# Performance work log

Hardware: AMD Instinct MI355X
Metric: run time of the kernel (lower is better)

## Reference

```python
import jax, jax.numpy as jnp
import numpy as np

Z_WHAT = 64      # z_what latent size
DEC = 64         # decoded object patch size
IMG = 128        # output canvas size (ssd_config.DATA.SHAPE[0])
HID = 1024       # what-decoder hidden size
FEATURE_MAPS = [4, 2, 1]
BOXES_PER_LOC = [2, 2, 2]
B = 16


def build_indices():
    # Faithful port of Decoder.reconstruction_indices
    idx = []
    img_idx = last = 0
    for fm, bpl in zip(FEATURE_MAPS, BOXES_PER_LOC):
        for f in range(fm * fm):
            img_idx = last + f
            idx.append(np.full(bpl, img_idx, dtype=np.int32))
        last = img_idx + 1
    return np.concatenate(idx)


def setup_inputs() -> dict:
    key = jax.random.key(0)
    ks = jax.random.split(key, 6)
    idx = build_indices()
    N = idx.shape[0]            # 42 boxes
    NL = int(idx.max()) + 1     # 21 locations
    z_present = jax.random.randint(ks[4], (B, N, 1), 0, 2, jnp.int32)
    z_present = z_present.at[:, 0, 0].set(1)  # ensure >=1 present per image
    return {
        "z_what": jax.random.normal(ks[0], (B, NL, Z_WHAT), jnp.float32),
        "z_where": jax.random.uniform(ks[1], (B, N, 4), jnp.float32, 0.05, 0.95),
        "z_depth": jax.random.normal(ks[2], (B, NL, 1), jnp.float32),
        "w1": jax.random.normal(ks[3], (Z_WHAT, HID), jnp.float32) * 0.05,
        "b1": jnp.zeros((HID,), jnp.float32),
        "w2": jax.random.normal(ks[5], (HID, 3 * DEC * DEC), jnp.float32) * 0.05,
        "b2": jnp.zeros((3 * DEC * DEC,), jnp.float32),
        "z_present": z_present,
        "indices": jnp.asarray(idx),
    }


def _sample_one(img, px, py):
    # Bilinear grid-sample (zeros padding, align_corners=False) of one
    # [3,S,S] patch at pixel coords px, py of shape [H,W].
    S = img.shape[-1]
    x0 = jnp.floor(px)
    y0 = jnp.floor(py)
    wx = px - x0
    wy = py - y0
    x0i = x0.astype(jnp.int32)
    y0i = y0.astype(jnp.int32)

    def gather(xi, yi):
        valid = (xi >= 0) & (xi < S) & (yi >= 0) & (yi < S)
        v = img[:, jnp.clip(yi, 0, S - 1), jnp.clip(xi, 0, S - 1)]
        return v * valid[None].astype(img.dtype)

    return (gather(x0i, y0i) * ((1 - wx) * (1 - wy))[None]
            + gather(x0i + 1, y0i) * (wx * (1 - wy))[None]
            + gather(x0i, y0i + 1) * ((1 - wx) * wy)[None]
            + gather(x0i + 1, y0i + 1) * (wx * wy)[None])


def _forward(z_what, z_where, z_depth, w1, b1, w2, b2, z_present, indices):
    Bb, NL, D = z_what.shape
    N = indices.shape[0]
    # index_select: expand per-location latents to per-box
    zw = jnp.take(z_what, indices, axis=1)          # [B,N,D]
    zd = jnp.take(z_depth, indices, axis=1)[..., 0]  # [B,N]

    # WhatDecoder: MLP -> sigmoid -> [B*N,3,DEC,DEC] object patches
    h = jax.nn.relu(zw.reshape(-1, D) @ w1 + b1)
    dec = jax.nn.sigmoid(h @ w2 + b2).reshape(-1, 3, DEC, DEC)

    # WhereTransformer: place each patch into IMG x IMG canvas via
    # inverse-affine STN from z_where = (cx, cy, w, h) in [0,1].
    zwf = z_where.reshape(-1, 4)
    cx, cy, w, hh = zwf[:, 0], zwf[:, 1], zwf[:, 2], zwf[:, 3]
    t = (jnp.arange(IMG, dtype=z_what.dtype) + 0.5) / IMG * 2.0 - 1.0
    xt = t[None, :]  # [1,IMG]
    yt = t[:, None]  # [IMG,1]
    xs = (xt[None] - (2 * cx - 1)[:, None, None]) / jnp.maximum(w, 1e-6)[:, None, None]
    ys = (yt[None] - (2 * cy - 1)[:, None, None]) / jnp.maximum(hh, 1e-6)[:, None, None]
    px = ((xs + 1) * DEC - 1) / 2  # [B*N,IMG,IMG]
    py = ((ys + 1) * DEC - 1) / 2
    trans = jax.vmap(_sample_one)(dec, px, py).reshape(Bb, N, 3, IMG, IMG)

    # Masked softmax over depth == padded softmax with -inf starter in the
    # original: absent objects get exactly zero merge weight.
    masked = jnp.where(z_present[..., 0] == 1, zd, -jnp.inf)
    wgt = jax.nn.softmax(masked, axis=1)  # [B,N]
    return jnp.einsum('bn,bnchw->bchw', wgt, trans)


def reference(z_what, z_where, z_depth, w1, b1, w2, b2, z_present, indices):
    return _forward(z_what, z_where, z_depth, w1, b1, w2, b2, z_present, indices)
```

## Files before the change

kernel.cpp:

```cpp
#include <hip/hip_runtime.h>

#define B_    16
#define NL    21
#define NG    42
#define ZW    64
#define HID   1024
#define DECW  64
#define IMG   128
#define NOUT  12288
#define MROWS 336
#define MPAD  384

typedef __bf16 bf16x8 __attribute__((ext_vector_type(8)));
typedef float f32x4 __attribute__((ext_vector_type(4)));
typedef unsigned short ushort8v __attribute__((ext_vector_type(8)));
typedef unsigned short ushort4v __attribute__((ext_vector_type(4)));

static __device__ __forceinline__ unsigned short f2bf(float f) {
    union { float f; unsigned int u; } v; v.f = f;
    unsigned int r = v.u + 0x7fffu + ((v.u >> 16) & 1u);
    return (unsigned short)(r >> 16);
}

__global__ __launch_bounds__(256) void k0_w2_transpose(const float* __restrict__ w2,
                                                       unsigned short* __restrict__ w2t) {
    __shared__ float tile[64][65];
    const int nt = blockIdx.x;
    const int kt = blockIdx.y;
    const int t  = threadIdx.x;
    const int n0 = nt * 64, k0 = kt * 64;
    #pragma unroll
    for (int i = 0; i < 4; ++i) {
        int lin = i * 256 + t;
        int kr  = lin >> 4;
        int nc  = (lin & 15) << 2;
        float4 v = *reinterpret_cast<const float4*>(w2 + (size_t)(k0 + kr) * NOUT + n0 + nc);
        tile[kr][nc + 0] = v.x; tile[kr][nc + 1] = v.y;
        tile[kr][nc + 2] = v.z; tile[kr][nc + 3] = v.w;
    }
    __syncthreads();
    #pragma unroll
    for (int i = 0; i < 4; ++i) {
        int lin = i * 256 + t;
        int nc  = lin >> 4;
        int kc  = (lin & 15) << 2;
        ushort4v r;
        r.x = f2bf(tile[kc + 0][nc]);
        r.y = f2bf(tile[kc + 1][nc]);
        r.z = f2bf(tile[kc + 2][nc]);
        r.w = f2bf(tile[kc + 3][nc]);
        *reinterpret_cast<ushort4v*>(w2t + (size_t)(n0 + nc) * HID + k0 + kc) = r;
    }
}

__global__ __launch_bounds__(256) void k1_h(const float* __restrict__ z_what,
                                            const float* __restrict__ w1,
                                            const float* __restrict__ b1,
                                            unsigned short* __restrict__ h) {
    const int r = blockIdx.x, t = threadIdx.x;
    if (r >= MROWS) {
        #pragma unroll
        for (int i = 0; i < 4; ++i) h[(size_t)r * HID + t + i * 256] = 0;
        return;
    }
    __shared__ float zs[ZW];
    if (t < ZW) zs[t] = z_what[(size_t)r * ZW + t];
    __syncthreads();
    float acc[4];
    #pragma unroll
    for (int i = 0; i < 4; ++i) acc[i] = b1[t + i * 256];
    for (int k = 0; k < ZW; ++k) {
        float z = zs[k];
        const float* wr = w1 + (size_t)k * HID + t;
        acc[0] = fmaf(z, wr[0],   acc[0]);
        acc[1] = fmaf(z, wr[256], acc[1]);
        acc[2] = fmaf(z, wr[512], acc[2]);
        acc[3] = fmaf(z, wr[768], acc[3]);
    }
    #pragma unroll
    for (int i = 0; i < 4; ++i)
        h[(size_t)r * HID + t + i * 256] = f2bf(acc[i] > 0.f ? acc[i] : 0.f);
}

__global__ void k3_params(const float* __restrict__ z_where,
                          const float* __restrict__ z_depth,
                          const int* __restrict__ z_present,
                          const int* __restrict__ indices,
                          float* __restrict__ params) {
    const int b = blockIdx.x, t = threadIdx.x;
    const bool valid = t < NG;
    int idx  = valid ? indices[t] : 0;
    int pres = valid ? z_present[b * NG + t] : 0;
    float zd = z_depth[b * NL + idx];
    const bool on = valid && (pres == 1);
    float val = on ? zd : -__builtin_inff();
    float m = val;
    #pragma unroll
    for (int off = 32; off; off >>= 1) m = fmaxf(m, __shfl_xor(m, off));
    float e = on ? __expf(val - m) : 0.f;
    float s = e;
    #pragma unroll
    for (int off = 32; off; off >>= 1) s += __shfl_xor(s, off);
    if (valid) {
        float wn = e / s;
        const float* zw = z_where + (size_t)(b * NG + t) * 4;
        float cx = zw[0], cy = zw[1], ww = zw[2], hh = zw[3];
        float wm = fmaxf(ww, 1e-6f), hm = fmaxf(hh, 1e-6f);
        float Ax = 32.f / wm, Ay = 32.f / hm;
        float Bx = 31.5f - (2.f * cx - 1.f) * Ax;
        float By = 31.5f - (2.f * cy - 1.f) * Ay;
        float* p = params + (size_t)(b * NG + t) * 8;
        p[0] = wn; p[1] = Ax; p[2] = Bx; p[3] = Ay; p[4] = By;
        p[5] = __int_as_float(b * NL + idx);
    }
}

__global__ __launch_bounds__(256) void k2_gemm(const unsigned short* __restrict__ h,
                                               const unsigned short* __restrict__ w2t,
                                               const float* __restrict__ b2,
                                               float* __restrict__ dec) {
    __shared__ unsigned short As[64 * 64];
    __shared__ unsigned short Bs[128 * 64];
    const int t    = threadIdx.x;
    const int bn   = blockIdx.x;
    const int bm   = blockIdx.y;
    const int row0 = bm * 64, col0 = bn * 128;
    const int lane = t & 63, wid = t >> 6;
    const int wr = (wid >> 1) * 32, wc = (wid & 1) * 64;

    f32x4 acc[2][4];
    const f32x4 zero = {0.f, 0.f, 0.f, 0.f};
    #pragma unroll
    for (int m = 0; m < 2; ++m)
        #pragma unroll
        for (int n = 0; n < 4; ++n) acc[m][n] = zero;

    for (int k0 = 0; k0 < HID; k0 += 64) {
        #pragma unroll
        for (int rnd = 0; rnd < 2; ++rnd) {
            int ci  = rnd * 256 + t;
            int row = ci >> 3;
            int bir = (ci & 7) << 4;
            ushort8v v = *reinterpret_cast<const ushort8v*>(
                h + (size_t)(row0 + row) * HID + k0 + (bir >> 1));
            int dst = row * 128 + (bir ^ ((row & 7) << 4));
            *reinterpret_cast<ushort8v*>(reinterpret_cast<char*>(As) + dst) = v;
        }
        #pragma unroll
        for (int rnd = 0; rnd < 4; ++rnd) {
            int ci  = rnd * 256 + t;
            int col = ci >> 3;
            int bir = (ci & 7) << 4;
            ushort8v v = *reinterpret_cast<const ushort8v*>(
                w2t + (size_t)(col0 + col) * HID + k0 + (bir >> 1));
            int dst = col * 128 + (bir ^ ((col & 7) << 4));
            *reinterpret_cast<ushort8v*>(reinterpret_cast<char*>(Bs) + dst) = v;
        }
        __syncthreads();
        #pragma unroll
        for (int ks = 0; ks < 2; ++ks) {
            const int kb = ks * 64 + ((lane >> 4) << 4);
            bf16x8 a[2], bb[4];
            #pragma unroll
            for (int m = 0; m < 2; ++m) {
                int row = wr + m * 16 + (lane & 15);
                int ad  = row * 128 + (kb ^ ((row & 7) << 4));
                a[m] = *reinterpret_cast<const bf16x8*>(reinterpret_cast<const char*>(As) + ad);
            }
            #pragma unroll
            for (int n = 0; n < 4; ++n) {
                int col = wc + n * 16 + (lane & 15);
                int ad  = col * 128 + (kb ^ ((col & 7) << 4));
                bb[n] = *reinterpret_cast<const bf16x8*>(reinterpret_cast<const char*>(Bs) + ad);
            }
            #pragma unroll
            for (int m = 0; m < 2; ++m)
                #pragma unroll
                for (int n = 0; n < 4; ++n)
                    acc[m][n] = __builtin_amdgcn_mfma_f32_16x16x32_bf16(a[m], bb[n], acc[m][n], 0, 0, 0);
        }
        __syncthreads();
    }
    const int rbase = row0 + wr + ((lane >> 4) << 2);
    const int cbase = col0 + wc + (lane & 15);
    #pragma unroll
    for (int n = 0; n < 4; ++n) {
        int col = cbase + n * 16;
        float bias = b2[col];
        #pragma unroll
        for (int m = 0; m < 2; ++m) {
            #pragma unroll
            for (int j = 0; j < 4; ++j) {
                int row = rbase + m * 16 + j;
                float v = acc[m][n][j] + bias;
                dec[(size_t)row * NOUT + col] = 1.f / (1.f + __expf(-v));
            }
        }
    }
}

__global__ __launch_bounds__(256) void k4_composite(const float* __restrict__ dec,
                                                    const float* __restrict__ params,
                                                    float* __restrict__ out) {
    __shared__ float P[NG * 6];
    const int b    = blockIdx.x >> 6;
    const int tile = blockIdx.x & 63;
    const int t    = threadIdx.x;
    if (t < NG * 6) {
        int n = t / 6, sl = t % 6;
        P[t] = params[(size_t)(b * NG + n) * 8 + sl];
    }
    __syncthreads();
    const int x = ((tile & 7) << 4) + (t & 15);
    const int y = ((tile >> 3) << 4) + (t >> 4);
    const float xt = (x + 0.5f) * (1.f / 64.f) - 1.f;
    const float yt = (y + 0.5f) * (1.f / 64.f) - 1.f;
    float a0 = 0.f, a1 = 0.f, a2 = 0.f;
    for (int n = 0; n < NG; ++n) {
        float wn = P[n * 6 + 0];
        if (wn == 0.f) continue;
        float px = fmaf(xt, P[n * 6 + 1], P[n * 6 + 2]);
        float py = fmaf(yt, P[n * 6 + 3], P[n * 6 + 4]);
        if (!(px > -1.f && px < 64.f && py > -1.f && py < 64.f)) continue;
        float x0f = floorf(px), y0f = floorf(py);
        float wx = px - x0f, wy = py - y0f;
        int x0 = (int)x0f, y0 = (int)y0f;
        int x1 = x0 + 1, y1 = y0 + 1;
        bool vx0 = x0 >= 0, vx1 = x1 < 64, vy0 = y0 >= 0, vy1 = y1 < 64;
        int ridx = __float_as_int(P[n * 6 + 5]);
        const float* base = dec + (size_t)ridx * NOUT;
        float w00 = (1.f - wx) * (1.f - wy), w10 = wx * (1.f - wy);
        float w01 = (1.f - wx) * wy,         w11 = wx * wy;
        int o00 = y0 * 64 + x0, o10 = y0 * 64 + x1;
        int o01 = y1 * 64 + x0, o11 = y1 * 64 + x1;
        #pragma unroll
        for (int c = 0; c < 3; ++c) {
            const float* cb = base + c * 4096;
            float v00 = (vx0 && vy0) ? cb[o00] : 0.f;
            float v10 = (vx1 && vy0) ? cb[o10] : 0.f;
            float v01 = (vx0 && vy1) ? cb[o01] : 0.f;
            float v11 = (vx1 && vy1) ? cb[o11] : 0.f;
            float s = v00 * w00 + v10 * w10 + v01 * w01 + v11 * w11;
            if      (c == 0) a0 = fmaf(wn, s, a0);
            else if (c == 1) a1 = fmaf(wn, s, a1);
            else             a2 = fmaf(wn, s, a2);
        }
    }
    out[((size_t)(b * 3 + 0) * IMG + y) * IMG + x] = a0;
    out[((size_t)(b * 3 + 1) * IMG + y) * IMG + x] = a1;
    out[((size_t)(b * 3 + 2) * IMG + y) * IMG + x] = a2;
}

extern "C" void kernel_launch(void* const* d_in, const int* in_sizes, int n_in,
                              void* d_out, int out_size, void* d_ws, size_t ws_size,
                              hipStream_t stream) {
    const float* z_what   = (const float*)d_in[0];
    const float* z_where  = (const float*)d_in[1];
    const float* z_depth  = (const float*)d_in[2];
    const float* w1       = (const float*)d_in[3];
    const float* b1       = (const float*)d_in[4];
    const float* w2       = (const float*)d_in[5];
    const float* b2       = (const float*)d_in[6];
    const int*   z_present= (const int*)d_in[7];
    const int*   indices  = (const int*)d_in[8];
    float* out = (float*)d_out;

    char* ws = (char*)d_ws;
    unsigned short* w2t = (unsigned short*)ws;
    unsigned short* h   = (unsigned short*)(ws + 25165824);
    float*          dec = (float*)(ws + 25165824 + 786432);
    float*       params = (float*)(ws + 25165824 + 786432 + 18874368);

    hipLaunchKernelGGL(k0_w2_transpose, dim3(192, 16), dim3(256), 0, stream, w2, w2t);
    hipLaunchKernelGGL(k1_h,            dim3(MPAD),    dim3(256), 0, stream, z_what, w1, b1, h);
    hipLaunchKernelGGL(k3_params,       dim3(B_),      dim3(64),  0, stream, z_where, z_depth, z_present, indices, params);
    hipLaunchKernelGGL(k2_gemm,         dim3(96, 6),   dim3(256), 0, stream, h, w2t, b2, dec);
    hipLaunchKernelGGL(k4_composite,    dim3(1024),    dim3(256), 0, stream, dec, params, out);
}
```

Baseline: 150.4 us.

## Double-buffer GEMM with direct global-to-LDS loads, pre-swizzle operands, cull composite objects

Operands are now written pre-swizzled in global memory: the transposed w2 and the hidden activations h use an XOR swizzle, so the GEMM can copy them straight into LDS with global_load_lds and no register round trip. The GEMM tile grows to 128x128 with a 4x4 MFMA accumulator per wave and double-buffered LDS stages, so the next k-tile loads while the current one is computed. The params kernel now also computes per-object pixel bounding boxes, and the composite kernel uses a ballot to compact only the objects that overlap each 16x16 tile. The trade-offs are a larger LDS footprint, fewer GEMM blocks (288), and added per-object setup work.

```diff
diff --git a/kernel.cpp b/kernel.cpp
--- a/kernel.cpp
+++ b/kernel.cpp
@@ -5,7 +5,6 @@
 #define NG    42
 #define ZW    64
 #define HID   1024
-#define DECW  64
 #define IMG   128
 #define NOUT  12288
 #define MROWS 336
@@ -20,6 +19,13 @@
     union { float f; unsigned int u; } v; v.f = f;
     unsigned int r = v.u + 0x7fffu + ((v.u >> 16) & 1u);
     return (unsigned short)(r >> 16);
+}
+
+static __device__ __forceinline__ void gload_lds16(const void* g, void* l) {
+    __builtin_amdgcn_global_load_lds(
+        (const __attribute__((address_space(1))) void*)g,
+        (__attribute__((address_space(3))) void*)l,
+        16, 0, 0);
 }
 
 __global__ __launch_bounds__(256) void k0_w2_transpose(const float* __restrict__ w2,
@@ -49,7 +55,8 @@
         r.y = f2bf(tile[kc + 1][nc]);
         r.z = f2bf(tile[kc + 2][nc]);
         r.w = f2bf(tile[kc + 3][nc]);
-        *reinterpret_cast<ushort4v*>(w2t + (size_t)(n0 + nc) * HID + k0 + kc) = r;
+        int kc_s = kc ^ ((nc & 7) << 3);
+        *reinterpret_cast<ushort4v*>(w2t + (size_t)(n0 + nc) * HID + k0 + kc_s) = r;
     }
 }
 
@@ -58,9 +65,13 @@
                                             const float* __restrict__ b1,
                                             unsigned short* __restrict__ h) {
     const int r = blockIdx.x, t = threadIdx.x;
+    const int sw = (r & 7) << 3;
     if (r >= MROWS) {
         #pragma unroll
-        for (int i = 0; i < 4; ++i) h[(size_t)r * HID + t + i * 256] = 0;
+        for (int i = 0; i < 4; ++i) {
+            int k = t + i * 256;
+            h[(size_t)r * HID + ((k & ~63) | ((k & 63) ^ sw))] = 0;
+        }
         return;
     }
     __shared__ float zs[ZW];
@@ -78,8 +89,11 @@
         acc[3] = fmaf(z, wr[768], acc[3]);
     }
     #pragma unroll
-    for (int i = 0; i < 4; ++i)
-        h[(size_t)r * HID + t + i * 256] = f2bf(acc[i] > 0.f ? acc[i] : 0.f);
+    for (int i = 0; i < 4; ++i) {
+        int k = t + i * 256;
+        h[(size_t)r * HID + ((k & ~63) | ((k & 63) ^ sw))] =
+            f2bf(acc[i] > 0.f ? acc[i] : 0.f);
+    }
 }
 
 __global__ void k3_params(const float* __restrict__ z_where,
@@ -109,9 +123,19 @@
         float Ax = 32.f / wm, Ay = 32.f / hm;
         float Bx = 31.5f - (2.f * cx - 1.f) * Ax;
         float By = 31.5f - (2.f * cy - 1.f) * Ay;
-        float* p = params + (size_t)(b * NG + t) * 8;
+        float xlof = ((-1.f - Bx) / Ax + 1.f) * 64.f - 0.5f;
+        float xhif = (( 64.f - Bx) / Ax + 1.f) * 64.f - 0.5f;
+        float ylof = ((-1.f - By) / Ay + 1.f) * 64.f - 0.5f;
+        float yhif = (( 64.f - By) / Ay + 1.f) * 64.f - 0.5f;
+        int xlo = max(0,   (int)floorf(xlof));
+        int xhi = min(128, (int)floorf(xhif) + 2);
+        int ylo = max(0,   (int)floorf(ylof));
+        int yhi = min(128, (int)floorf(yhif) + 2);
+        float* p = params + (size_t)(b * NG + t) * 16;
         p[0] = wn; p[1] = Ax; p[2] = Bx; p[3] = Ay; p[4] = By;
         p[5] = __int_as_float(b * NL + idx);
+        p[6] = __int_as_float(xlo); p[7] = __int_as_float(xhi);
+        p[8] = __int_as_float(ylo); p[9] = __int_as_float(yhi);
     }
 }
 
@@ -119,68 +143,80 @@
                                                const unsigned short* __restrict__ w2t,
                                                const float* __restrict__ b2,
                                                float* __restrict__ dec) {
-    __shared__ unsigned short As[64 * 64];
-    __shared__ unsigned short Bs[128 * 64];
+    __shared__ char smem[65536];
     const int t    = threadIdx.x;
     const int bn   = blockIdx.x;
     const int bm   = blockIdx.y;
-    const int row0 = bm * 64, col0 = bn * 128;
+    const int row0 = bm * 128, col0 = bn * 128;
     const int lane = t & 63, wid = t >> 6;
-    const int wr = (wid >> 1) * 32, wc = (wid & 1) * 64;
-
-    f32x4 acc[2][4];
+    const int wr = (wid >> 1) * 64, wc = (wid & 1) * 64;
+
+    f32x4 acc[4][4];
     const f32x4 zero = {0.f, 0.f, 0.f, 0.f};
     #pragma unroll
-    for (int m = 0; m < 2; ++m)
+    for (int m = 0; m < 4; ++m)
         #pragma unroll
         for (int n = 0; n < 4; ++n) acc[m][n] = zero;
 
-    for (int k0 = 0; k0 < HID; k0 += 64) {
-        #pragma unroll
-        for (int rnd = 0; rnd < 2; ++rnd) {
-            int ci  = rnd * 256 + t;
-            int row = ci >> 3;
-            int bir = (ci & 7) << 4;
-            ushort8v v = *reinterpret_cast<const ushort8v*>(
-                h + (size_t)(row0 + row) * HID + k0 + (bir >> 1));
-            int dst = row * 128 + (bir ^ ((row & 7) << 4));
-            *reinterpret_cast<ushort8v*>(reinterpret_cast<char*>(As) + dst) = v;
-        }
-        #pragma unroll
-        for (int rnd = 0; rnd < 4; ++rnd) {
-            int ci  = rnd * 256 + t;
-            int col = ci >> 3;
-            int bir = (ci & 7) << 4;
-            ushort8v v = *reinterpret_cast<const ushort8v*>(
-                w2t + (size_t)(col0 + col) * HID + k0 + (bir >> 1));
-            int dst = col * 128 + (bir ^ ((col & 7) << 4));
-            *reinterpret_cast<ushort8v*>(reinterpret_cast<char*>(Bs) + dst) = v;
-        }
+    const char* hB = (const char*)h   + ((size_t)row0 << 11);
+    const char* wB = (const char*)w2t + ((size_t)col0 << 11);
+
+    #define STAGE(kt_, buf_)                                                        \
+        do {                                                                        \
+            int kby = (kt_) << 7;                                    \
+            char* ldsA = smem + (buf_) * 32768;                                     \
+            char* ldsB = ldsA + 16384;                                              \
+            _Pragma("unroll")                                                       \
+            for (int r_ = 0; r_ < 4; ++r_) {                                        \
+                int ci  = r_ * 256 + t;                                             \
+                int row = ci >> 3, kc = ci & 7;                                     \
+                gload_lds16(hB + ((size_t)row << 11) + kby + (kc << 4),             \
+                            ldsA + ci * 16);                                        \
+                gload_lds16(wB + ((size_t)row << 11) + kby + (kc << 4),             \
+                            ldsB + ci * 16);                                        \
+            }                                                                       \
+        } while (0)
+
+    #define COMPUTE(buf_)                                                           \
+        do {                                                                        \
+            const char* Ab = smem + (buf_) * 32768;                                 \
+            const char* Bb = Ab + 16384;                                            \
+            _Pragma("unroll")                                                       \
+            for (int ks = 0; ks < 2; ++ks) {                                        \
+                int kb = ks * 64 + ((lane >> 4) << 4);                              \
+                bf16x8 a[4], bb[4];                                                 \
+                _Pragma("unroll")                                                   \
+                for (int m = 0; m < 4; ++m) {                                       \
+                    int row = wr + m * 16 + (lane & 15);                            \
+                    a[m] = *reinterpret_cast<const bf16x8*>(                        \
+                        Ab + row * 128 + (kb ^ ((row & 7) << 4)));                  \
+                }                                                                   \
+                _Pragma("unroll")                                                   \
+                for (int n = 0; n < 4; ++n) {                                       \
+                    int col = wc + n * 16 + (lane & 15);                            \
+                    bb[n] = *reinterpret_cast<const bf16x8*>(                       \
+                        Bb + col * 128 + (kb ^ ((col & 7) << 4)));                  \
+                }                                                                   \
+                _Pragma("unroll")                                                   \
+                for (int m = 0; m < 4; ++m)                                         \
+                    _Pragma("unroll")                                               \
+                    for (int n = 0; n < 4; ++n)                                     \
+                        acc[m][n] = __builtin_amdgcn_mfma_f32_16x16x32_bf16(        \
+                            a[m], bb[n], acc[m][n], 0, 0, 0);                       \
+            }                                                                       \
+        } while (0)
+
+    STAGE(0, 0);
+    __syncthreads();
+    int cur = 0;
+    for (int kt = 1; kt < 16; ++kt) {
+        STAGE(kt, cur ^ 1);
+        COMPUTE(cur);
         __syncthreads();
-        #pragma unroll
-        for (int ks = 0; ks < 2; ++ks) {
-            const int kb = ks * 64 + ((lane >> 4) << 4);
-            bf16x8 a[2], bb[4];
-            #pragma unroll
-            for (int m = 0; m < 2; ++m) {
-                int row = wr + m * 16 + (lane & 15);
-                int ad  = row * 128 + (kb ^ ((row & 7) << 4));
-                a[m] = *reinterpret_cast<const bf16x8*>(reinterpret_cast<const char*>(As) + ad);
-            }
-            #pragma unroll
-            for (int n = 0; n < 4; ++n) {
-                int col = wc + n * 16 + (lane & 15);
-                int ad  = col * 128 + (kb ^ ((col & 7) << 4));
-                bb[n] = *reinterpret_cast<const bf16x8*>(reinterpret_cast<const char*>(Bs) + ad);
-            }
-            #pragma unroll
-            for (int m = 0; m < 2; ++m)
-                #pragma unroll
-                for (int n = 0; n < 4; ++n)
-                    acc[m][n] = __builtin_amdgcn_mfma_f32_16x16x32_bf16(a[m], bb[n], acc[m][n], 0, 0, 0);
-        }
-        __syncthreads();
-    }
+        cur ^= 1;
+    }
+    COMPUTE(cur);
+
     const int rbase = row0 + wr + ((lane >> 4) << 2);
     const int cbase = col0 + wc + (lane & 15);
     #pragma unroll
@@ -188,7 +224,7 @@
         int col = cbase + n * 16;
         float bias = b2[col];
         #pragma unroll
-        for (int m = 0; m < 2; ++m) {
+        for (int m = 0; m < 4; ++m) {
             #pragma unroll
             for (int j = 0; j < 4; ++j) {
                 int row = rbase + m * 16 + j;
@@ -197,37 +233,60 @@
             }
         }
     }
+    #undef STAGE
+    #undef COMPUTE
 }
 
 __global__ __launch_bounds__(256) void k4_composite(const float* __restrict__ dec,
                                                     const float* __restrict__ params,
                                                     float* __restrict__ out) {
-    __shared__ float P[NG * 6];
+    __shared__ float Pc[NG * 6];
+    __shared__ int s_cnt;
     const int b    = blockIdx.x >> 6;
     const int tile = blockIdx.x & 63;
+    const int tx0 = (tile & 7) << 4, ty0 = (tile >> 3) << 4;
     const int t    = threadIdx.x;
-    if (t < NG * 6) {
-        int n = t / 6, sl = t % 6;
-        P[t] = params[(size_t)(b * NG + n) * 8 + sl];
+    if (t < 64) {
+        bool pass = false;
+        float wn = 0.f, Ax = 0.f, Bx = 0.f, Ay = 0.f, By = 0.f, ridx = 0.f;
+        if (t < NG) {
+            const float* p = params + (size_t)(b * NG + t) * 16;
+            wn = p[0];
+            if (wn != 0.f) {
+                int xlo = __float_as_int(p[6]), xhi = __float_as_int(p[7]);
+                int ylo = __float_as_int(p[8]), yhi = __float_as_int(p[9]);
+                if (xlo < tx0 + 16 && xhi > tx0 && ylo < ty0 + 16 && yhi > ty0) {
+                    pass = true; Ax = p[1]; Bx = p[2]; Ay = p[3]; By = p[4]; ridx = p[5];
+                }
+            }
+        }
+        unsigned long long mask = __ballot(pass);
+        if (pass) {
+            int slot = __popcll(mask & ((1ull << t) - 1ull));
+            float* q = Pc + slot * 6;
+            q[0] = wn; q[1] = Ax; q[2] = Bx; q[3] = Ay; q[4] = By; q[5] = ridx;
+        }
+        if (t == 0) s_cnt = __popcll(mask);
     }
     __syncthreads();
-    const int x = ((tile & 7) << 4) + (t & 15);
-    const int y = ((tile >> 3) << 4) + (t >> 4);
+    const int cnt = s_cnt;
+    const int x = tx0 + (t & 15);
+    const int y = ty0 + (t >> 4);
     const float xt = (x + 0.5f) * (1.f / 64.f) - 1.f;
     const float yt = (y + 0.5f) * (1.f / 64.f) - 1.f;
     float a0 = 0.f, a1 = 0.f, a2 = 0.f;
-    for (int n = 0; n < NG; ++n) {
-        float wn = P[n * 6 + 0];
-        if (wn == 0.f) continue;
-        float px = fmaf(xt, P[n * 6 + 1], P[n * 6 + 2]);
-        float py = fmaf(yt, P[n * 6 + 3], P[n * 6 + 4]);
+    for (int i = 0; i < cnt; ++i) {
+        const float* q = Pc + i * 6;
+        float wn = q[0];
+        float px = fmaf(xt, q[1], q[2]);
+        float py = fmaf(yt, q[3], q[4]);
         if (!(px > -1.f && px < 64.f && py > -1.f && py < 64.f)) continue;
         float x0f = floorf(px), y0f = floorf(py);
         float wx = px - x0f, wy = py - y0f;
         int x0 = (int)x0f, y0 = (int)y0f;
         int x1 = x0 + 1, y1 = y0 + 1;
         bool vx0 = x0 >= 0, vx1 = x1 < 64, vy0 = y0 >= 0, vy1 = y1 < 64;
-        int ridx = __float_as_int(P[n * 6 + 5]);
+        int ridx = __float_as_int(q[5]);
         const float* base = dec + (size_t)ridx * NOUT;
         float w00 = (1.f - wx) * (1.f - wy), w10 = wx * (1.f - wy);
         float w01 = (1.f - wx) * wy,         w11 = wx * wy;
@@ -240,10 +299,10 @@
             float v10 = (vx1 && vy0) ? cb[o10] : 0.f;
             float v01 = (vx0 && vy1) ? cb[o01] : 0.f;
             float v11 = (vx1 && vy1) ? cb[o11] : 0.f;
-            float s = v00 * w00 + v10 * w10 + v01 * w01 + v11 * w11;
-            if      (c == 0) a0 = fmaf(wn, s, a0);
-            else if (c == 1) a1 = fmaf(wn, s, a1);
-            else             a2 = fmaf(wn, s, a2);
+            float sv = v00 * w00 + v10 * w10 + v01 * w01 + v11 * w11;
+            if      (c == 0) a0 = fmaf(wn, sv, a0);
+            else if (c == 1) a1 = fmaf(wn, sv, a1);
+            else             a2 = fmaf(wn, sv, a2);
         }
     }
     out[((size_t)(b * 3 + 0) * IMG + y) * IMG + x] = a0;
@@ -274,6 +333,6 @@
     hipLaunchKernelGGL(k0_w2_transpose, dim3(192, 16), dim3(256), 0, stream, w2, w2t);
     hipLaunchKernelGGL(k1_h,            dim3(MPAD),    dim3(256), 0, stream, z_what, w1, b1, h);
     hipLaunchKernelGGL(k3_params,       dim3(B_),      dim3(64),  0, stream, z_where, z_depth, z_present, indices, params);
-    hipLaunchKernelGGL(k2_gemm,         dim3(96, 6),   dim3(256), 0, stream, h, w2t, b2, dec);
+    hipLaunchKernelGGL(k2_gemm,         dim3(96, 3),   dim3(256), 0, stream, h, w2t, b2, dec);
     hipLaunchKernelGGL(k4_composite,    dim3(1024),    dim3(256), 0, stream, dec, params, out);
 }
```

New measurement: 145.3 us. -3.4%, faster.
